# Kernel optimization log

Measured on AMD Instinct MI355X. Metric: run time of the kernel, lower is better.

## Reference

```python
import jax, jax.numpy as jnp
import numpy as np

B, L, D = 2, 2048, 2048
H = 16
DH = D // H  # 128
EPS = 1e-6


def _rope_cos_sin(seq_len, dim, dtype):
    inv_freq = 1.0 / (10000.0 ** (jnp.arange(0, dim, 2, dtype=jnp.float32) / dim))
    t = jnp.arange(seq_len, dtype=jnp.float32)
    freqs = jnp.einsum('i,j->ij', t, inv_freq)          # [L, dim/2]
    emb = jnp.concatenate([freqs, freqs], axis=-1)      # [L, dim]
    return jnp.cos(emb).astype(dtype)[None, None], jnp.sin(emb).astype(dtype)[None, None]


def _rotate_half(x):
    x1, x2 = jnp.split(x, 2, axis=-1)
    return jnp.concatenate([-x2, x1], axis=-1)


def _rms_norm(x, w):
    var = jnp.mean(jnp.square(x), axis=-1, keepdims=True)
    return x * jax.lax.rsqrt(var + EPS) * w


def setup_inputs() -> dict:
    key = jax.random.key(0)
    ks = jax.random.split(key, 4)
    s_in = 1.0 / np.sqrt(D)
    return {
        'x': jax.random.normal(ks[0], (B, L, D), jnp.float32),
        'attention_mask': jnp.zeros((B, 1, 1, L), jnp.bool_),
        'Wqkv': jax.random.normal(ks[1], (D, 3 * D), jnp.float32) * s_in,
        'bqkv': jnp.zeros((3 * D,), jnp.float32),
        'Wout': jax.random.normal(ks[2], (D, D), jnp.float32) * s_in,
        'bout': jnp.zeros((D,), jnp.float32),
        'q_norm_w': jnp.ones((DH,), jnp.float32),
        'k_norm_w': jnp.ones((DH,), jnp.float32),
    }


def reference(x, attention_mask, Wqkv, bqkv, Wout, bout, q_norm_w, k_norm_w):
    b, l, d = x.shape
    qkv = x @ Wqkv + bqkv                                   # [B,L,3D]
    q, k, v = jnp.split(qkv, 3, axis=-1)
    # [B,H,L,DH]
    q = q.reshape(b, l, H, DH).transpose(0, 2, 1, 3)
    k = k.reshape(b, l, H, DH).transpose(0, 2, 1, 3)
    v = v.reshape(b, l, H, DH).transpose(0, 2, 1, 3)

    cos, sin = _rope_cos_sin(l, DH, x.dtype)
    q = q * cos + _rotate_half(q) * sin
    k = k * cos + _rotate_half(k) * sin

    q = _rms_norm(q, q_norm_w)
    k = _rms_norm(k, k_norm_w)

    # SDPA with additive (float-cast) mask, as in the original code
    scale = 1.0 / np.sqrt(DH)
    scores = jnp.einsum('bhqd,bhkd->bhqk', q, k) * scale
    scores = scores + attention_mask.astype(x.dtype)        # broadcast [B,1,1,L]
    attn = jax.nn.softmax(scores, axis=-1)
    out = jnp.einsum('bhqk,bhkd->bhqd', attn, v)            # [B,H,L,DH]

    # zero out masked query rows: padding_mask = mask.transpose(2,3) -> [B,1,L,1]
    padding_mask = jnp.swapaxes(attention_mask, 2, 3)
    out = jnp.where(padding_mask, 0.0, out)

    out = out.transpose(0, 2, 1, 3).reshape(b, l, d)
    return out @ Wout + bout
```

## Files before the change

kernel.cpp:

```cpp
#include <hip/hip_runtime.h>
#include <hip/hip_bf16.h>

typedef __bf16 bf16;
using bf16x8 = __attribute__((ext_vector_type(8))) __bf16;
using bf16x4 = __attribute__((ext_vector_type(4))) __bf16;
using f32x4  = __attribute__((ext_vector_type(4))) float;
using f32x16 = __attribute__((ext_vector_type(16))) float;

#define DEV __device__ __forceinline__

DEV void load_lds16(const void* g, void* l) {
  __builtin_amdgcn_global_load_lds(
      (const __attribute__((address_space(1))) void*)g,
      (__attribute__((address_space(3))) void*)l, 16, 0, 0);
}

__global__ void k_tab(float* __restrict__ ct, float* __restrict__ st) {
  int l = blockIdx.x, i = threadIdx.x;
  double invf = pow(10000.0, -(double)i / 64.0);
  double a = (double)l * invf;
  ct[l * 64 + i] = (float)cos(a);
  st[l * 64 + i] = (float)sin(a);
}

__global__ void k_f2b(const float* __restrict__ in, bf16* __restrict__ out, long n) {
  long i = ((long)blockIdx.x * blockDim.x + threadIdx.x) * 8;
  if (i >= n) return;
  float4 a = *(const float4*)(in + i);
  float4 b = *(const float4*)(in + i + 4);
  bf16x8 o;
  o[0] = (bf16)a.x; o[1] = (bf16)a.y; o[2] = (bf16)a.z; o[3] = (bf16)a.w;
  o[4] = (bf16)b.x; o[5] = (bf16)b.y; o[6] = (bf16)b.z; o[7] = (bf16)b.w;
  *(bf16x8*)(out + i) = o;
}

__global__ __launch_bounds__(256) void k_tconv(const float* __restrict__ in,
                                               bf16* __restrict__ out, int R, int C) {
  __shared__ float t[64][65];
  int nbc = C >> 6;
  long r0 = (long)(blockIdx.x / nbc) * 64, c0 = (long)(blockIdx.x % nbc) * 64;
  int tid = threadIdx.x;
#pragma unroll
  for (int i = 0; i < 4; ++i) {
    int ch = tid + i * 256;
    int r = ch >> 4, c4 = (ch & 15) * 4;
    float4 v = *(const float4*)(in + (r0 + r) * C + c0 + c4);
    t[r][c4] = v.x; t[r][c4 + 1] = v.y; t[r][c4 + 2] = v.z; t[r][c4 + 3] = v.w;
  }
  __syncthreads();
#pragma unroll
  for (int i = 0; i < 2; ++i) {
    int ch = tid + i * 256;
    int c = ch >> 3, r8 = (ch & 7) * 8;
    bf16x8 o;
#pragma unroll
    for (int j = 0; j < 8; ++j) o[j] = (bf16)t[r8 + j][c];
    *(bf16x8*)(out + (c0 + c) * R + r0 + r8) = o;
  }
}

template <typename OutT>
__global__ __launch_bounds__(256) void k_gemm_bt(
    const bf16* __restrict__ A, const bf16* __restrict__ Bt,
    const float* __restrict__ bias, OutT* __restrict__ C,
    int M, int N, int K) {
  __shared__ __align__(16) bf16 lA[128 * 32];
  __shared__ __align__(16) bf16 lB[128 * 32];
  int bid = blockIdx.x;
  if ((gridDim.x & 7) == 0) {
    int q = gridDim.x >> 3;
    bid = (bid & 7) * q + (bid >> 3);
  }
  int nbn = N >> 7;
  int bm = bid / nbn, bn = bid % nbn;
  const int tid = threadIdx.x, lane = tid & 63, wid = tid >> 6;
  const int wr = wid >> 1, wc = wid & 1;
  const int fr = lane & 15, fq = lane >> 4;
  const long abase = (long)bm * 128 * K, bbase = (long)bn * 128 * K;
  f32x4 acc[4][4] = {};

  for (int k0 = 0; k0 < K; k0 += 32) {
    __syncthreads();
#pragma unroll
    for (int it = 0; it < 2; ++it) {
      int ch = wid * 128 + it * 64 + lane;
      int r = ch >> 2, c = (ch & 3) * 8;
      load_lds16(A + abase + (long)r * K + k0 + c, &lA[(wid * 128 + it * 64) * 8]);
    }
#pragma unroll
    for (int it = 0; it < 2; ++it) {
      int ch = wid * 128 + it * 64 + lane;
      int r = ch >> 2, c = (ch & 3) * 8;
      load_lds16(Bt + bbase + (long)r * K + k0 + c, &lB[(wid * 128 + it * 64) * 8]);
    }
    __syncthreads();
    bf16x8 af[4], bfr[4];
#pragma unroll
    for (int m = 0; m < 4; ++m) af[m] = *(const bf16x8*)&lA[(wr * 64 + m * 16 + fr) * 32 + fq * 8];
#pragma unroll
    for (int n = 0; n < 4; ++n) bfr[n] = *(const bf16x8*)&lB[(wc * 64 + n * 16 + fr) * 32 + fq * 8];
#pragma unroll
    for (int m = 0; m < 4; ++m)
#pragma unroll
      for (int n = 0; n < 4; ++n)
        acc[m][n] = __builtin_amdgcn_mfma_f32_16x16x32_bf16(af[m], bfr[n], acc[m][n], 0, 0, 0);
  }
#pragma unroll
  for (int n = 0; n < 4; ++n) {
    int col = bn * 128 + wc * 64 + n * 16 + fr;
    float bv = bias[col];
#pragma unroll
    for (int m = 0; m < 4; ++m) {
      int row0 = bm * 128 + wr * 64 + m * 16 + fq * 4;
#pragma unroll
      for (int r = 0; r < 4; ++r) {
        float v = acc[m][n][r] + bv;
        C[(long)(row0 + r) * N + col] = (OutT)v;
      }
    }
  }
}

__global__ __launch_bounds__(256) void k_qkpost(
    const bf16* __restrict__ qkv, const float* __restrict__ ct, const float* __restrict__ st,
    const float* __restrict__ qw, const float* __restrict__ kw,
    bf16* __restrict__ q_r, bf16* __restrict__ k_r) {
  int bl = blockIdx.x;
  int l = bl & 2047;
  int b = bl >> 11;
  int tid = threadIdx.x;
  int h = tid >> 4, i8 = (tid & 15) * 8;
  bool lo = i8 < 64;
  float c[8], s[8];
#pragma unroll
  for (int j = 0; j < 8; ++j) {
    int d = (i8 + j) & 63;
    c[j] = ct[l * 64 + d];
    s[j] = st[l * 64 + d];
  }
#pragma unroll
  for (int part = 0; part < 2; ++part) {
    bf16x8 xv = *(const bf16x8*)(qkv + (long)bl * 6144 + part * 2048 + h * 128 + i8);
    float v[8], p[8], r[8];
    float ss = 0.f;
#pragma unroll
    for (int j = 0; j < 8; ++j) v[j] = (float)xv[j];
#pragma unroll
    for (int j = 0; j < 8; ++j) p[j] = __shfl_xor(v[j], 8);
#pragma unroll
    for (int j = 0; j < 8; ++j) {
      r[j] = lo ? v[j] * c[j] - p[j] * s[j] : v[j] * c[j] + p[j] * s[j];
      ss += r[j] * r[j];
    }
    ss += __shfl_xor(ss, 1);
    ss += __shfl_xor(ss, 2);
    ss += __shfl_xor(ss, 4);
    ss += __shfl_xor(ss, 8);
    float inv = rsqrtf(ss * (1.f / 128.f) + 1e-6f);
    const float* wv = part ? kw : qw;
    bf16* dst = (part ? k_r : q_r) + ((long)(b * 16 + h) * 2048 + l) * 128 + i8;
    bf16x8 ov;
#pragma unroll
    for (int j = 0; j < 8; ++j) ov[j] = (bf16)(r[j] * inv * wv[i8 + j]);
    *(bf16x8*)dst = ov;
  }
}

__global__ __launch_bounds__(256) void k_vt(const bf16* __restrict__ qkv, bf16* __restrict__ v_t) {
  __shared__ bf16 t[64][130];
  int blk = blockIdx.x;
  int lt = blk & 31, bh = blk >> 5;
  int b = bh >> 4, h = bh & 15;
  int l0 = lt * 64;
  int tid = threadIdx.x;
#pragma unroll
  for (int i = 0; i < 4; ++i) {
    int ch = tid + i * 256;
    int r = ch >> 4, c8 = (ch & 15) * 8;
    bf16x8 v = *(const bf16x8*)(qkv + (long)(b * 2048 + l0 + r) * 6144 + 4096 + h * 128 + c8);
#pragma unroll
    for (int j = 0; j < 8; ++j) t[r][c8 + j] = v[j];
  }
  __syncthreads();
#pragma unroll
  for (int i = 0; i < 4; ++i) {
    int ch = tid + i * 256;
    int d = ch >> 3, l8 = (ch & 7) * 8;
    bf16x8 o;
#pragma unroll
    for (int j = 0; j < 8; ++j) o[j] = t[l8 + j][d];
    *(bf16x8*)(v_t + ((long)bh * 128 + d) * 2048 + l0 + l8) = o;
  }
}

__global__ __launch_bounds__(512, 2) void k_attn(
    const bf16* __restrict__ q_r, const bf16* __restrict__ k_r,
    const bf16* __restrict__ v_t, const unsigned char* __restrict__ amask,
    bf16* __restrict__ attno) {
  __shared__ __align__(16) bf16 lK[2][64 * 128];
  __shared__ __align__(16) bf16 lV[2][128 * 64];
  __shared__ float lRow[8 * 32];
  const int tid = threadIdx.x, lane = tid & 63, w = tid >> 6;
  const int hi = lane >> 5, q31 = lane & 31;
  const int qt = blockIdx.x & 7, bh = blockIdx.x >> 3;
  const int b = bh >> 4, h = bh & 15;
  const long hbase = (long)bh * 2048 * 128;
  const int q0 = qt * 256 + w * 32;
  const unsigned char* mb = amask + b * 2048;

  bf16x8 qf[8];
#pragma unroll
  for (int ksl = 0; ksl < 8; ++ksl)
    qf[ksl] = *(const bf16x8*)(q_r + hbase + (long)(q0 + q31) * 128 + ksl * 16 + hi * 8);

  f32x16 o[4] = {};
  float m_run = -1e30f, l_run = 0.f;
  const float SC2 = 0.08838834764831845f * 1.4426950408889634f;
  const float L2E = 1.4426950408889634f;

#define STAGE(buf, kv0)                                                              \
  {                                                                                  \
    _Pragma("unroll") for (int it = 0; it < 2; ++it) {                               \
      int g = it * 512 + w * 64 + lane;                                              \
      int r = g >> 4, u = g & 15;                                                    \
      load_lds16(k_r + hbase + (long)((kv0) + r) * 128 + ((u ^ (r & 7)) << 3),       \
                 &lK[buf][(it * 512 + w * 64) * 8]);                                 \
    }                                                                                \
    _Pragma("unroll") for (int it = 0; it < 2; ++it) {                               \
      int g = it * 512 + w * 64 + lane;                                              \
      int r = g >> 3, u = g & 7;                                                     \
      load_lds16(v_t + hbase + (long)r * 2048 + (kv0) + ((u ^ (r & 7)) << 3),        \
                 &lV[buf][(it * 512 + w * 64) * 8]);                                 \
    }                                                                                \
  }

  STAGE(0, 0);
  __syncthreads();
  int cur = 0;
  for (int t = 0; t < 32; ++t) {
    const int kv0 = t << 6;
    if (t < 31) STAGE(cur ^ 1, kv0 + 64);

    f32x16 st0 = {}, st1 = {};
#pragma unroll
    for (int ksl = 0; ksl < 8; ++ksl) {
      const int u = ksl * 2 + hi;
      bf16x8 kf0 = *(const bf16x8*)&lK[cur][q31 * 128 + ((u ^ (q31 & 7)) << 3)];
      bf16x8 kf1 = *(const bf16x8*)&lK[cur][(32 + q31) * 128 + ((u ^ (q31 & 7)) << 3)];
      st0 = __builtin_amdgcn_mfma_f32_32x32x16_bf16(kf0, qf[ksl], st0, 0, 0, 0);
      st1 = __builtin_amdgcn_mfma_f32_32x32x16_bf16(kf1, qf[ksl], st1, 0, 0, 0);
    }

    unsigned long long anym = __ballot(mb[kv0 + lane] != 0);
#pragma unroll
    for (int i = 0; i < 16; ++i) { st0[i] *= SC2; st1[i] *= SC2; }
    if (anym) {
#pragma unroll
      for (int i = 0; i < 16; ++i) {
        int c = (i & 3) + 8 * (i >> 2) + 4 * hi;
        if (mb[kv0 + c]) st0[i] += L2E;
        if (mb[kv0 + 32 + c]) st1[i] += L2E;
      }
    }

    float tm = st0[0];
#pragma unroll
    for (int i = 1; i < 16; ++i) tm = fmaxf(tm, st0[i]);
#pragma unroll
    for (int i = 0; i < 16; ++i) tm = fmaxf(tm, st1[i]);
    tm = fmaxf(tm, __shfl_xor(tm, 32));

    if (!__all(tm <= m_run + 8.f)) {
      float mn = fmaxf(m_run, tm);
      float corr = exp2f(m_run - mn);
      m_run = mn;
      l_run *= corr;
      if (hi == 0) lRow[w * 32 + q31] = corr;
      asm volatile("s_waitcnt lgkmcnt(0)" ::: "memory");
#pragma unroll
      for (int i = 0; i < 16; ++i) {
        float cr = lRow[w * 32 + (i & 3) + 8 * (i >> 2) + 4 * hi];
#pragma unroll
        for (int dt = 0; dt < 4; ++dt) o[dt][i] *= cr;
      }
    }

    float rs = 0.f;
#pragma unroll
    for (int i = 0; i < 16; ++i) { st0[i] = exp2f(st0[i] - m_run); rs += st0[i]; }
#pragma unroll
    for (int i = 0; i < 16; ++i) { st1[i] = exp2f(st1[i] - m_run); rs += st1[i]; }
    rs += __shfl_xor(rs, 32);
    l_run += rs;

    union UU { bf16x4 v; uint2 u; };
    union U8 { bf16x8 v; uint4 u; };
    bf16x8 pa[4];
#define MKPA(pidx, STX, bb)                                                          \
  {                                                                                  \
    UU plo, phi;                                                                     \
    plo.v = (bf16x4){(bf16)STX[bb], (bf16)STX[(bb) + 1], (bf16)STX[(bb) + 2],        \
                     (bf16)STX[(bb) + 3]};                                           \
    phi.v = (bf16x4){(bf16)STX[(bb) + 4], (bf16)STX[(bb) + 5], (bf16)STX[(bb) + 6],  \
                     (bf16)STX[(bb) + 7]};                                           \
    unsigned sx = hi ? plo.u.x : phi.u.x, sy = hi ? plo.u.y : phi.u.y;               \
    unsigned rx = (unsigned)__shfl_xor((int)sx, 32), ry = (unsigned)__shfl_xor((int)sy, 32); \
    U8 f;                                                                            \
    f.u.x = hi ? rx : plo.u.x; f.u.y = hi ? ry : plo.u.y;                            \
    f.u.z = hi ? phi.u.x : rx; f.u.w = hi ? phi.u.y : ry;                            \
    pa[pidx] = f.v;                                                                  \
  }
    MKPA(0, st0, 0) MKPA(1, st0, 8) MKPA(2, st1, 0) MKPA(3, st1, 8)
#undef MKPA

#pragma unroll
    for (int dt = 0; dt < 4; ++dt) {
      const int dr = dt * 32 + q31;
#pragma unroll
      for (int ks = 0; ks < 4; ++ks) {
        const int u = ks * 2 + hi;
        bf16x8 vb = *(const bf16x8*)&lV[cur][dr * 64 + ((u ^ (dr & 7)) << 3)];
        o[dt] = __builtin_amdgcn_mfma_f32_32x32x16_bf16(pa[ks], vb, o[dt], 0, 0, 0);
      }
    }

    __syncthreads();
    cur ^= 1;
  }
#undef STAGE

  if (hi == 0) lRow[w * 32 + q31] = 1.f / l_run;
  asm volatile("s_waitcnt lgkmcnt(0)" ::: "memory");
#pragma unroll
  for (int i = 0; i < 16; ++i) {
    int q = (i & 3) + 8 * (i >> 2) + 4 * hi;
    int qrow = q0 + q;
    float inv = lRow[w * 32 + q];
    float zm = mb[qrow] ? 0.f : inv;
#pragma unroll
    for (int dt = 0; dt < 4; ++dt)
      attno[(long)(b * 2048 + qrow) * 2048 + h * 128 + dt * 32 + q31] = (bf16)(o[dt][i] * zm);
  }
}

extern "C" void kernel_launch(void* const* d_in, const int* in_sizes, int n_in,
                              void* d_out, int out_size, void* d_ws, size_t ws_size,
                              hipStream_t stream) {
  const float* x = (const float*)d_in[0];
  const unsigned char* amask = (const unsigned char*)d_in[1];
  const float* Wqkv = (const float*)d_in[2];
  const float* bqkv = (const float*)d_in[3];
  const float* Wout = (const float*)d_in[4];
  const float* bout = (const float*)d_in[5];
  const float* qw = (const float*)d_in[6];
  const float* kw = (const float*)d_in[7];
  float* out = (float*)d_out;
  char* ws = (char*)d_ws;

  bf16* xb   = (bf16*)(ws);
  bf16* wqT  = (bf16*)(ws + 16777216);
  bf16* woT  = (bf16*)(ws + 41943040);
  bf16* qkv  = (bf16*)(ws + 50331648);
  bf16* q_r  = (bf16*)(ws + 100663296);
  bf16* k_r  = (bf16*)(ws + 117440512);
  bf16* v_t  = (bf16*)(ws + 134217728);
  float* ct  = (float*)(ws + 150994944);
  float* st  = ct + 2048 * 64;
  bf16* attno = xb;

  k_tab<<<2048, 64, 0, stream>>>(ct, st);
  k_f2b<<<4096, 256, 0, stream>>>(x, xb, 8388608L);
  k_tconv<<<32 * 96, 256, 0, stream>>>(Wqkv, wqT, 2048, 6144);
  k_tconv<<<32 * 32, 256, 0, stream>>>(Wout, woT, 2048, 2048);
  k_gemm_bt<bf16><<<32 * 48, 256, 0, stream>>>(xb, wqT, bqkv, qkv, 4096, 6144, 2048);
  k_qkpost<<<4096, 256, 0, stream>>>(qkv, ct, st, qw, kw, q_r, k_r);
  k_vt<<<1024, 256, 0, stream>>>(qkv, v_t);
  k_attn<<<256, 512, 0, stream>>>(q_r, k_r, v_t, amask, attno);
  k_gemm_bt<float><<<32 * 16, 256, 0, stream>>>(attno, woT, bout, out, 4096, 2048, 2048);
}
```

Baseline: 348.9 us.

## Rewrite GEMM with double-buffered LDS, swizzled layout, and larger 128x256 tiles

Replaces the single-buffered 128x128x32 GEMM with a 512-thread kernel using 128x256 tiles and K-step 64. It prefetches two stages ahead through global_load_lds, paced by explicit vmcnt waits and barriers. An XOR swizzle on LDS columns reduces bank conflicts, and s_setprio raises priority around the MFMA bursts. The goal is to hide global load latency and raise arithmetic intensity for both projection GEMMs. The costs are more LDS (96KB per block, which limits residency) and fewer blocks for the output GEMM (256 tiles).

```diff
diff --git a/kernel.cpp b/kernel.cpp
--- a/kernel.cpp
+++ b/kernel.cpp
@@ -60,63 +60,100 @@
 }
 
 template <typename OutT>
-__global__ __launch_bounds__(256) void k_gemm_bt(
+__global__ __launch_bounds__(512, 2) void k_gemm2(
     const bf16* __restrict__ A, const bf16* __restrict__ Bt,
     const float* __restrict__ bias, OutT* __restrict__ C,
     int M, int N, int K) {
-  __shared__ __align__(16) bf16 lA[128 * 32];
-  __shared__ __align__(16) bf16 lB[128 * 32];
-  int bid = blockIdx.x;
-  if ((gridDim.x & 7) == 0) {
+  __shared__ __align__(16) bf16 lA[2][128 * 64];
+  __shared__ __align__(16) bf16 lB[2][256 * 64];
+  const int nbm = M >> 7;
+  int swz = blockIdx.x;
+  {
     int q = gridDim.x >> 3;
-    bid = (bid & 7) * q + (bid >> 3);
-  }
-  int nbn = N >> 7;
-  int bm = bid / nbn, bn = bid % nbn;
-  const int tid = threadIdx.x, lane = tid & 63, wid = tid >> 6;
-  const int wr = wid >> 1, wc = wid & 1;
+    swz = (swz & 7) * q + (swz >> 3);
+  }
+  const int bm = swz % nbm, bn = swz / nbm;
+  const int tid = threadIdx.x, lane = tid & 63, w = tid >> 6;
+  const int wm = w >> 2, wn = w & 3;
   const int fr = lane & 15, fq = lane >> 4;
-  const long abase = (long)bm * 128 * K, bbase = (long)bn * 128 * K;
+  const long abase = (long)bm * 128 * K;
+  const long bbase = (long)bn * 256 * K;
+  const int NT = K >> 6;
   f32x4 acc[4][4] = {};
 
-  for (int k0 = 0; k0 < K; k0 += 32) {
-    __syncthreads();
-#pragma unroll
-    for (int it = 0; it < 2; ++it) {
-      int ch = wid * 128 + it * 64 + lane;
-      int r = ch >> 2, c = (ch & 3) * 8;
-      load_lds16(A + abase + (long)r * K + k0 + c, &lA[(wid * 128 + it * 64) * 8]);
-    }
-#pragma unroll
-    for (int it = 0; it < 2; ++it) {
-      int ch = wid * 128 + it * 64 + lane;
-      int r = ch >> 2, c = (ch & 3) * 8;
-      load_lds16(Bt + bbase + (long)r * K + k0 + c, &lB[(wid * 128 + it * 64) * 8]);
-    }
-    __syncthreads();
-    bf16x8 af[4], bfr[4];
-#pragma unroll
-    for (int m = 0; m < 4; ++m) af[m] = *(const bf16x8*)&lA[(wr * 64 + m * 16 + fr) * 32 + fq * 8];
-#pragma unroll
-    for (int n = 0; n < 4; ++n) bfr[n] = *(const bf16x8*)&lB[(wc * 64 + n * 16 + fr) * 32 + fq * 8];
+#define STAGE2(d, k0)                                                        \
+  {                                                                          \
+    _Pragma("unroll") for (int ld = 0; ld < 2; ++ld) {                       \
+      int g = ld * 512 + w * 64 + lane;                                      \
+      int r = g >> 3, u = g & 7;                                             \
+      load_lds16(A + abase + (long)r * K + (k0) + ((u ^ (r & 7)) << 3),      \
+                 &lA[d][(ld * 512 + w * 64) * 8]);                           \
+    }                                                                        \
+    _Pragma("unroll") for (int ld = 0; ld < 4; ++ld) {                       \
+      int g = ld * 512 + w * 64 + lane;                                      \
+      int r = g >> 3, u = g & 7;                                             \
+      load_lds16(Bt + bbase + (long)r * K + (k0) + ((u ^ (r & 7)) << 3),     \
+                 &lB[d][(ld * 512 + w * 64) * 8]);                           \
+    }                                                                        \
+  }
+
+  STAGE2(0, 0)
+  STAGE2(1, 64)
+  asm volatile("s_waitcnt vmcnt(6)" ::: "memory");
+  __builtin_amdgcn_s_barrier();
+
+  for (int t = 0; t < NT; ++t) {
+    const int d = t & 1;
+    bf16x8 af[4][2];
 #pragma unroll
     for (int m = 0; m < 4; ++m)
 #pragma unroll
-      for (int n = 0; n < 4; ++n)
-        acc[m][n] = __builtin_amdgcn_mfma_f32_16x16x32_bf16(af[m], bfr[n], acc[m][n], 0, 0, 0);
-  }
+      for (int kk = 0; kk < 2; ++kk) {
+        int r = wm * 64 + m * 16 + fr;
+        af[m][kk] = *(const bf16x8*)&lA[d][r * 64 + (((kk * 4 + fq) ^ (r & 7)) << 3)];
+      }
+#pragma unroll
+    for (int nh = 0; nh < 2; ++nh) {
+      bf16x8 bfx[2][2];
+#pragma unroll
+      for (int n = 0; n < 2; ++n)
+#pragma unroll
+        for (int kk = 0; kk < 2; ++kk) {
+          int r = wn * 64 + nh * 32 + n * 16 + fr;
+          bfx[n][kk] = *(const bf16x8*)&lB[d][r * 64 + (((kk * 4 + fq) ^ (r & 7)) << 3)];
+        }
+      __builtin_amdgcn_s_setprio(1);
+#pragma unroll
+      for (int m = 0; m < 4; ++m)
+#pragma unroll
+        for (int n = 0; n < 2; ++n)
+#pragma unroll
+          for (int kk = 0; kk < 2; ++kk)
+            acc[m][nh * 2 + n] = __builtin_amdgcn_mfma_f32_16x16x32_bf16(
+                af[m][kk], bfx[n][kk], acc[m][nh * 2 + n], 0, 0, 0);
+      __builtin_amdgcn_s_setprio(0);
+    }
+    __builtin_amdgcn_s_barrier();
+    if (t + 2 < NT) {
+      STAGE2(d, (t + 2) << 6)
+      asm volatile("s_waitcnt vmcnt(6)" ::: "memory");
+    } else {
+      asm volatile("s_waitcnt vmcnt(0)" ::: "memory");
+    }
+    __builtin_amdgcn_s_barrier();
+  }
+#undef STAGE2
+
 #pragma unroll
   for (int n = 0; n < 4; ++n) {
-    int col = bn * 128 + wc * 64 + n * 16 + fr;
+    int col = bn * 256 + wn * 64 + n * 16 + fr;
     float bv = bias[col];
 #pragma unroll
     for (int m = 0; m < 4; ++m) {
-      int row0 = bm * 128 + wr * 64 + m * 16 + fq * 4;
-#pragma unroll
-      for (int r = 0; r < 4; ++r) {
-        float v = acc[m][n][r] + bv;
-        C[(long)(row0 + r) * N + col] = (OutT)v;
-      }
+      int row0 = bm * 128 + wm * 64 + m * 16 + fq * 4;
+#pragma unroll
+      for (int r = 0; r < 4; ++r)
+        C[(long)(row0 + r) * N + col] = (OutT)(acc[m][n][r] + bv);
     }
   }
 }
@@ -372,9 +409,9 @@
   k_f2b<<<4096, 256, 0, stream>>>(x, xb, 8388608L);
   k_tconv<<<32 * 96, 256, 0, stream>>>(Wqkv, wqT, 2048, 6144);
   k_tconv<<<32 * 32, 256, 0, stream>>>(Wout, woT, 2048, 2048);
-  k_gemm_bt<bf16><<<32 * 48, 256, 0, stream>>>(xb, wqT, bqkv, qkv, 4096, 6144, 2048);
+  k_gemm2<bf16><<<768, 512, 0, stream>>>(xb, wqT, bqkv, qkv, 4096, 6144, 2048);
   k_qkpost<<<4096, 256, 0, stream>>>(qkv, ct, st, qw, kw, q_r, k_r);
   k_vt<<<1024, 256, 0, stream>>>(qkv, v_t);
   k_attn<<<256, 512, 0, stream>>>(q_r, k_r, v_t, amask, attno);
-  k_gemm_bt<float><<<32 * 16, 256, 0, stream>>>(attno, woT, bout, out, 4096, 2048, 2048);
-}
+  k_gemm2<float><<<256, 512, 0, stream>>>(attno, woT, bout, out, 4096, 2048, 2048);
+}
```

Measured after the change: 367.0 us. 5.2% more time.

## Rewrite GEMM as 256x256-tile, 8-wave kernel with 4-stage async LDS pipeline

Applied to the files above, without the earlier changes.

Replaces the 128x128 single-buffered bf16 GEMM with a 256x256 tile computed by 8 waves. It uses a 4-slot LDS ring fed by global_load_lds three K-steps ahead, with manual vmcnt waits, XOR-swizzled LDS addressing to avoid bank conflicts, and setprio around MFMA bursts. The goal is to overlap global loads with MFMA work and to raise data reuse per loaded byte. The cost is large LDS use (128KB per block), which leaves few blocks per CU. Only 128 blocks are launched for the output projection, which may underfill the GPU's CUs.

```diff
diff --git a/kernel.cpp b/kernel.cpp
--- a/kernel.cpp
+++ b/kernel.cpp
@@ -60,63 +60,91 @@
 }
 
 template <typename OutT>
-__global__ __launch_bounds__(256) void k_gemm_bt(
+__global__ __launch_bounds__(512, 2) void k_gemm8(
     const bf16* __restrict__ A, const bf16* __restrict__ Bt,
     const float* __restrict__ bias, OutT* __restrict__ C,
     int M, int N, int K) {
-  __shared__ __align__(16) bf16 lA[128 * 32];
-  __shared__ __align__(16) bf16 lB[128 * 32];
-  int bid = blockIdx.x;
-  if ((gridDim.x & 7) == 0) {
-    int q = gridDim.x >> 3;
-    bid = (bid & 7) * q + (bid >> 3);
-  }
-  int nbn = N >> 7;
-  int bm = bid / nbn, bn = bid % nbn;
-  const int tid = threadIdx.x, lane = tid & 63, wid = tid >> 6;
-  const int wr = wid >> 1, wc = wid & 1;
+  __shared__ __align__(16) bf16 lA[4][256 * 32];
+  __shared__ __align__(16) bf16 lB[4][256 * 32];
+  const int nbm = M >> 8;
+  int swz = blockIdx.x;
+  { int q = gridDim.x >> 3; swz = (swz & 7) * q + (swz >> 3); }
+  const int bm = swz % nbm, bn = swz / nbm;
+  const int tid = threadIdx.x, lane = tid & 63, w = tid >> 6;
+  const int wm = w >> 2, wn = w & 3;
   const int fr = lane & 15, fq = lane >> 4;
-  const long abase = (long)bm * 128 * K, bbase = (long)bn * 128 * K;
-  f32x4 acc[4][4] = {};
-
-  for (int k0 = 0; k0 < K; k0 += 32) {
-    __syncthreads();
-#pragma unroll
-    for (int it = 0; it < 2; ++it) {
-      int ch = wid * 128 + it * 64 + lane;
-      int r = ch >> 2, c = (ch & 3) * 8;
-      load_lds16(A + abase + (long)r * K + k0 + c, &lA[(wid * 128 + it * 64) * 8]);
-    }
-#pragma unroll
-    for (int it = 0; it < 2; ++it) {
-      int ch = wid * 128 + it * 64 + lane;
-      int r = ch >> 2, c = (ch & 3) * 8;
-      load_lds16(Bt + bbase + (long)r * K + k0 + c, &lB[(wid * 128 + it * 64) * 8]);
-    }
-    __syncthreads();
-    bf16x8 af[4], bfr[4];
-#pragma unroll
-    for (int m = 0; m < 4; ++m) af[m] = *(const bf16x8*)&lA[(wr * 64 + m * 16 + fr) * 32 + fq * 8];
-#pragma unroll
-    for (int n = 0; n < 4; ++n) bfr[n] = *(const bf16x8*)&lB[(wc * 64 + n * 16 + fr) * 32 + fq * 8];
-#pragma unroll
-    for (int m = 0; m < 4; ++m)
-#pragma unroll
-      for (int n = 0; n < 4; ++n)
-        acc[m][n] = __builtin_amdgcn_mfma_f32_16x16x32_bf16(af[m], bfr[n], acc[m][n], 0, 0, 0);
-  }
-#pragma unroll
-  for (int n = 0; n < 4; ++n) {
-    int col = bn * 128 + wc * 64 + n * 16 + fr;
+  const long abase = (long)bm * 256 * K;
+  const long bbase = (long)bn * 256 * K;
+  const int NU = K >> 5;
+  f32x4 acc[8][4] = {};
+
+#define STG(GP, gbase, LARR, uu)                                                   \
+  { _Pragma("unroll") for (int it = 0; it < 2; ++it) {                             \
+      int g = it * 512 + w * 64 + lane;                                            \
+      int r = g >> 2, c = g & 3;                                                   \
+      load_lds16(GP + gbase + (long)r * K + ((uu) << 5) + ((c ^ ((r >> 1) & 3)) << 3), \
+                 &LARR[(uu) & 3][(it * 512 + w * 64) * 8]); } }
+
+  STG(A, abase, lA, 0) STG(Bt, bbase, lB, 0)
+  STG(A, abase, lA, 1) STG(Bt, bbase, lB, 1)
+  STG(A, abase, lA, 2) STG(Bt, bbase, lB, 2)
+
+  for (int u = 0; u < NU; ++u) {
+    const int sl = u & 3;
+    if (u < NU - 2)       asm volatile("s_waitcnt vmcnt(8)" ::: "memory");
+    else if (u == NU - 2) asm volatile("s_waitcnt vmcnt(4)" ::: "memory");
+    else                  asm volatile("s_waitcnt vmcnt(0)" ::: "memory");
+    __builtin_amdgcn_s_barrier();
+
+    bf16x8 af0[4], bfr[4];
+#pragma unroll
+    for (int i = 0; i < 4; ++i) {
+      int R = wm * 128 + i * 16 + fr;
+      af0[i] = *(const bf16x8*)&lA[sl][R * 32 + ((fq ^ ((R >> 1) & 3)) << 3)];
+      int Rb = wn * 64 + i * 16 + fr;
+      bfr[i] = *(const bf16x8*)&lB[sl][Rb * 32 + ((fq ^ ((Rb >> 1) & 3)) << 3)];
+    }
+    if (u + 3 < NU) { STG(A, abase, lA, u + 3) }
+    __builtin_amdgcn_s_barrier();
+    asm volatile("s_waitcnt lgkmcnt(0)" ::: "memory");
+    __builtin_amdgcn_s_setprio(1);
+#pragma unroll
+    for (int mb = 0; mb < 4; ++mb)
+#pragma unroll
+      for (int nb = 0; nb < 4; ++nb)
+        acc[mb][nb] = __builtin_amdgcn_mfma_f32_16x16x32_bf16(af0[mb], bfr[nb], acc[mb][nb], 0, 0, 0);
+    __builtin_amdgcn_s_setprio(0);
+    __builtin_amdgcn_s_barrier();
+
+    bf16x8 af1[4];
+#pragma unroll
+    for (int i = 0; i < 4; ++i) {
+      int R = wm * 128 + 64 + i * 16 + fr;
+      af1[i] = *(const bf16x8*)&lA[sl][R * 32 + ((fq ^ ((R >> 1) & 3)) << 3)];
+    }
+    if (u + 3 < NU) { STG(Bt, bbase, lB, u + 3) }
+    __builtin_amdgcn_s_barrier();
+    asm volatile("s_waitcnt lgkmcnt(0)" ::: "memory");
+    __builtin_amdgcn_s_setprio(1);
+#pragma unroll
+    for (int mb = 0; mb < 4; ++mb)
+#pragma unroll
+      for (int nb = 0; nb < 4; ++nb)
+        acc[4 + mb][nb] = __builtin_amdgcn_mfma_f32_16x16x32_bf16(af1[mb], bfr[nb], acc[4 + mb][nb], 0, 0, 0);
+    __builtin_amdgcn_s_setprio(0);
+  }
+#undef STG
+
+#pragma unroll
+  for (int nb = 0; nb < 4; ++nb) {
+    int col = bn * 256 + wn * 64 + nb * 16 + fr;
     float bv = bias[col];
 #pragma unroll
-    for (int m = 0; m < 4; ++m) {
-      int row0 = bm * 128 + wr * 64 + m * 16 + fq * 4;
-#pragma unroll
-      for (int r = 0; r < 4; ++r) {
-        float v = acc[m][n][r] + bv;
-        C[(long)(row0 + r) * N + col] = (OutT)v;
-      }
+    for (int mi = 0; mi < 8; ++mi) {
+      int row0 = bm * 256 + wm * 128 + (mi >> 2) * 64 + (mi & 3) * 16 + fq * 4;
+#pragma unroll
+      for (int r = 0; r < 4; ++r)
+        C[(long)(row0 + r) * N + col] = (OutT)(acc[mi][nb][r] + bv);
     }
   }
 }
@@ -372,9 +400,9 @@
   k_f2b<<<4096, 256, 0, stream>>>(x, xb, 8388608L);
   k_tconv<<<32 * 96, 256, 0, stream>>>(Wqkv, wqT, 2048, 6144);
   k_tconv<<<32 * 32, 256, 0, stream>>>(Wout, woT, 2048, 2048);
-  k_gemm_bt<bf16><<<32 * 48, 256, 0, stream>>>(xb, wqT, bqkv, qkv, 4096, 6144, 2048);
+  k_gemm8<bf16><<<384, 512, 0, stream>>>(xb, wqT, bqkv, qkv, 4096, 6144, 2048);
   k_qkpost<<<4096, 256, 0, stream>>>(qkv, ct, st, qw, kw, q_r, k_r);
   k_vt<<<1024, 256, 0, stream>>>(qkv, v_t);
   k_attn<<<256, 512, 0, stream>>>(q_r, k_r, v_t, amask, attno);
-  k_gemm_bt<float><<<32 * 16, 256, 0, stream>>>(attno, woT, bout, out, 4096, 2048, 2048);
-}
+  k_gemm8<float><<<128, 512, 0, stream>>>(attno, woT, bout, out, 4096, 2048, 2048);
+}
```

Measured after the change: 360.9 us. 1.03x slower.

## Double GEMM K-step with swizzled LDS; precompute mask flag and use shuffles in attention

Applied to the files above, without the earlier changes.

The GEMM now stages 64-wide K slices per iteration with an XOR-swizzled LDS layout. This halves the barrier count per K, doubles the MFMA work between syncs and avoids bank conflicts on fragment reads. The attention kernel checks the whole mask once per block instead of issuing a ballot per tile. It also replaces the LDS round-trips for the rescale factor and the final normalization with wave shuffles. The larger LDS footprint may lower GEMM occupancy.

```diff
diff --git a/kernel.cpp b/kernel.cpp
--- a/kernel.cpp
+++ b/kernel.cpp
@@ -64,8 +64,8 @@
     const bf16* __restrict__ A, const bf16* __restrict__ Bt,
     const float* __restrict__ bias, OutT* __restrict__ C,
     int M, int N, int K) {
-  __shared__ __align__(16) bf16 lA[128 * 32];
-  __shared__ __align__(16) bf16 lB[128 * 32];
+  __shared__ __align__(16) bf16 lA[128 * 64];
+  __shared__ __align__(16) bf16 lB[128 * 64];
   int bid = blockIdx.x;
   if ((gridDim.x & 7) == 0) {
     int q = gridDim.x >> 3;
@@ -79,31 +79,44 @@
   const long abase = (long)bm * 128 * K, bbase = (long)bn * 128 * K;
   f32x4 acc[4][4] = {};
 
-  for (int k0 = 0; k0 < K; k0 += 32) {
+  for (int k0 = 0; k0 < K; k0 += 64) {
     __syncthreads();
 #pragma unroll
-    for (int it = 0; it < 2; ++it) {
-      int ch = wid * 128 + it * 64 + lane;
-      int r = ch >> 2, c = (ch & 3) * 8;
-      load_lds16(A + abase + (long)r * K + k0 + c, &lA[(wid * 128 + it * 64) * 8]);
-    }
-#pragma unroll
-    for (int it = 0; it < 2; ++it) {
-      int ch = wid * 128 + it * 64 + lane;
-      int r = ch >> 2, c = (ch & 3) * 8;
-      load_lds16(Bt + bbase + (long)r * K + k0 + c, &lB[(wid * 128 + it * 64) * 8]);
+    for (int it = 0; it < 4; ++it) {
+      int ch = it * 256 + tid;
+      int r = ch >> 3, u = ch & 7;
+      load_lds16(A + abase + (long)r * K + k0 + ((u ^ (r & 7)) << 3), &lA[ch * 8]);
+    }
+#pragma unroll
+    for (int it = 0; it < 4; ++it) {
+      int ch = it * 256 + tid;
+      int r = ch >> 3, u = ch & 7;
+      load_lds16(Bt + bbase + (long)r * K + k0 + ((u ^ (r & 7)) << 3), &lB[ch * 8]);
     }
     __syncthreads();
-    bf16x8 af[4], bfr[4];
-#pragma unroll
-    for (int m = 0; m < 4; ++m) af[m] = *(const bf16x8*)&lA[(wr * 64 + m * 16 + fr) * 32 + fq * 8];
-#pragma unroll
-    for (int n = 0; n < 4; ++n) bfr[n] = *(const bf16x8*)&lB[(wc * 64 + n * 16 + fr) * 32 + fq * 8];
+    bf16x8 af[4][2], bf_[4][2];
+#pragma unroll
+    for (int m = 0; m < 4; ++m) {
+      int R = wr * 64 + m * 16 + fr;
+#pragma unroll
+      for (int kk = 0; kk < 2; ++kk)
+        af[m][kk] = *(const bf16x8*)&lA[R * 64 + (((kk * 4 + fq) ^ (R & 7)) << 3)];
+    }
+#pragma unroll
+    for (int n = 0; n < 4; ++n) {
+      int R = wc * 64 + n * 16 + fr;
+#pragma unroll
+      for (int kk = 0; kk < 2; ++kk)
+        bf_[n][kk] = *(const bf16x8*)&lB[R * 64 + (((kk * 4 + fq) ^ (R & 7)) << 3)];
+    }
 #pragma unroll
     for (int m = 0; m < 4; ++m)
 #pragma unroll
       for (int n = 0; n < 4; ++n)
-        acc[m][n] = __builtin_amdgcn_mfma_f32_16x16x32_bf16(af[m], bfr[n], acc[m][n], 0, 0, 0);
+#pragma unroll
+        for (int kk = 0; kk < 2; ++kk)
+          acc[m][n] = __builtin_amdgcn_mfma_f32_16x16x32_bf16(af[m][kk], bf_[n][kk],
+                                                              acc[m][n], 0, 0, 0);
   }
 #pragma unroll
   for (int n = 0; n < 4; ++n) {
@@ -199,7 +212,7 @@
     bf16* __restrict__ attno) {
   __shared__ __align__(16) bf16 lK[2][64 * 128];
   __shared__ __align__(16) bf16 lV[2][128 * 64];
-  __shared__ float lRow[8 * 32];
+  __shared__ int sAny;
   const int tid = threadIdx.x, lane = tid & 63, w = tid >> 6;
   const int hi = lane >> 5, q31 = lane & 31;
   const int qt = blockIdx.x & 7, bh = blockIdx.x >> 3;
@@ -207,6 +220,13 @@
   const long hbase = (long)bh * 2048 * 128;
   const int q0 = qt * 256 + w * 32;
   const unsigned char* mb = amask + b * 2048;
+
+  if (tid == 0) sAny = 0;
+  __syncthreads();
+  {
+    unsigned mv = *(const unsigned*)(mb + tid * 4);
+    if (mv) sAny = 1;
+  }
 
   bf16x8 qf[8];
 #pragma unroll
@@ -236,6 +256,7 @@
 
   STAGE(0, 0);
   __syncthreads();
+  const bool maskAny = sAny != 0;
   int cur = 0;
   for (int t = 0; t < 32; ++t) {
     const int kv0 = t << 6;
@@ -251,10 +272,9 @@
       st1 = __builtin_amdgcn_mfma_f32_32x32x16_bf16(kf1, qf[ksl], st1, 0, 0, 0);
     }
 
-    unsigned long long anym = __ballot(mb[kv0 + lane] != 0);
 #pragma unroll
     for (int i = 0; i < 16; ++i) { st0[i] *= SC2; st1[i] *= SC2; }
-    if (anym) {
+    if (maskAny) {
 #pragma unroll
       for (int i = 0; i < 16; ++i) {
         int c = (i & 3) + 8 * (i >> 2) + 4 * hi;
@@ -275,11 +295,9 @@
       float corr = exp2f(m_run - mn);
       m_run = mn;
       l_run *= corr;
-      if (hi == 0) lRow[w * 32 + q31] = corr;
-      asm volatile("s_waitcnt lgkmcnt(0)" ::: "memory");
 #pragma unroll
       for (int i = 0; i < 16; ++i) {
-        float cr = lRow[w * 32 + (i & 3) + 8 * (i >> 2) + 4 * hi];
+        float cr = __shfl(corr, (i & 3) + 8 * (i >> 2) + 4 * hi);
 #pragma unroll
         for (int dt = 0; dt < 4; ++dt) o[dt][i] *= cr;
       }
@@ -329,14 +347,14 @@
   }
 #undef STAGE
 
-  if (hi == 0) lRow[w * 32 + q31] = 1.f / l_run;
-  asm volatile("s_waitcnt lgkmcnt(0)" ::: "memory");
+  float invl = 1.f / l_run;
 #pragma unroll
   for (int i = 0; i < 16; ++i) {
     int q = (i & 3) + 8 * (i >> 2) + 4 * hi;
     int qrow = q0 + q;
-    float inv = lRow[w * 32 + q];
-    float zm = mb[qrow] ? 0.f : inv;
+    float inv = __shfl(invl, q);
+    float zm = inv;
+    if (maskAny) { if (mb[qrow]) zm = 0.f; }
 #pragma unroll
     for (int dt = 0; dt < 4; ++dt)
       attno[(long)(b * 2048 + qrow) * 2048 + h * 128 + dt * 32 + q31] = (bf16)(o[dt][i] * zm);
```

Measured after the change: 329.8 us. 5.5% less time.
